# Kernel optimization log

Measured on AMD Instinct MI355X. Metric: run time of the kernel, lower is better.

Reference implementation:

```python
import jax, jax.numpy as jnp
import numpy as np

VOCAB, E, H, L, B, T, S, V = 32000, 512, 1024, 2, 64, 64, 128, 1024
LSTM_IN = 2 * E  # input_feed=True -> cat(embed, prev_output)


def setup_inputs() -> dict:
    key = jax.random.key(0)
    ks = jax.random.split(key, 12)
    s = lambda *d: 1.0 / np.sqrt(d[-1])
    return {
        "tgt_batch": jax.random.randint(ks[0], (T, B), 0, VOCAB),
        "h_encoder": jax.random.normal(ks[1], (B, S, V), jnp.float32),
        "emb": jax.random.normal(ks[2], (VOCAB, E), jnp.float32) * 0.02,
        "output_init": jnp.zeros((B, E), jnp.float32),
        "hidden_init": jnp.zeros((L, B, H), jnp.float32),
        "W_ih": jax.random.uniform(ks[3], (L, 4 * H, LSTM_IN), jnp.float32, -s(H), s(H)),
        "W_hh": jax.random.uniform(ks[4], (L, 4 * H, H), jnp.float32, -s(H), s(H)),
        "b_ih": jax.random.uniform(ks[5], (L, 4 * H), jnp.float32, -s(H), s(H)),
        "b_hh": jax.random.uniform(ks[6], (L, 4 * H), jnp.float32, -s(H), s(H)),
        "W1": jax.random.uniform(ks[7], (V, H), jnp.float32, -s(H), s(H)),   # query_size->values_size
        "b1": jnp.zeros((V,), jnp.float32),
        "W2": jax.random.uniform(ks[8], (E, H + V), jnp.float32, -s(H + V), s(H + V)),
        "b2": jnp.zeros((E,), jnp.float32),
    }


def reference(tgt_batch, h_encoder, emb, output_init, hidden_init,
              W_ih, W_hh, b_ih, b_hh, W1, b1, W2, b2):
    x_seq = emb[tgt_batch]  # [T, B, E]

    def lstm_cell(x, h, c):  # x:[B,2E], h/c:[L,B,H]
        hs, cs, inp = [], [], x
        for l in range(L):
            gates = inp @ W_ih[l].T + b_ih[l] + h[l] @ W_hh[l].T + b_hh[l]
            i, f, g, o = jnp.split(gates, 4, axis=-1)  # torch gate order i,f,g,o
            c_new = jax.nn.sigmoid(f) * c[l] + jax.nn.sigmoid(i) * jnp.tanh(g)
            h_new = jax.nn.sigmoid(o) * jnp.tanh(c_new)
            hs.append(h_new); cs.append(c_new); inp = h_new
        return jnp.stack(hs), jnp.stack(cs), inp

    def global_attn(query):  # query:[B,H]
        q = query @ W1.T + b1                              # [B,V]
        scores = jnp.einsum('bv,bsv->bs', q, h_encoder)    # [B,S]
        a = jax.nn.softmax(scores, axis=-1)
        attended = jnp.einsum('bs,bsv->bv', a, h_encoder)  # [B,V]
        return jnp.tanh(jnp.concatenate([attended, query], axis=-1) @ W2.T + b2)

    def step(carry, x):
        h, c, out = carry
        inp = jnp.concatenate([x, out], axis=-1)  # input feed
        h, c, top = lstm_cell(inp, h, c)
        o = global_attn(top)  # dropout is identity in eval mode
        return (h, c, o), o

    c0 = jnp.zeros_like(hidden_init)
    _, outs = jax.lax.scan(step, (hidden_init, c0, output_init), x_seq)
    return jnp.transpose(outs, (1, 0, 2))  # [B, T, E]
```

## Files before the change

kernel.cpp:

```cpp
#include <hip/hip_runtime.h>

typedef _Float16 f16;
typedef f16 f16x8 __attribute__((ext_vector_type(8)));
typedef f16 f16x2 __attribute__((ext_vector_type(2)));
typedef float f32x4 __attribute__((ext_vector_type(4)));
typedef unsigned long long u64;

#define MFMA16(a, b, c) __builtin_amdgcn_mfma_f32_16x16x32_f16(a, b, c, 0, 0, 0)
#define ROT 16

__device__ inline float fsig(float x) { return 1.f / (1.f + __expf(-x)); }
__device__ inline float ftanh(float x) {
    x = fminf(15.f, fmaxf(-15.f, x));
    float e = __expf(2.f * x);
    return (e - 1.f) / (e + 1.f);
}

__device__ __forceinline__ void bstore8(void* p, u64 v) {
    __hip_atomic_store((u64*)p, v, __ATOMIC_RELAXED, __HIP_MEMORY_SCOPE_AGENT);
}
__device__ __forceinline__ void bstore4(float* p, float v) {
    __hip_atomic_store(p, v, __ATOMIC_RELAXED, __HIP_MEMORY_SCOPE_AGENT);
}
__device__ __forceinline__ float bload_f32(const float* p) {
    return __hip_atomic_load((float*)p, __ATOMIC_RELAXED, __HIP_MEMORY_SCOPE_AGENT);
}

__global__ __launch_bounds__(256) void k_convert(
    const float* __restrict__ Wih, const float* __restrict__ Whh,
    const float* __restrict__ W1, const float* __restrict__ W2,
    const float* __restrict__ bih, const float* __restrict__ bhh,
    const int* __restrict__ tgt, const float* __restrict__ emb,
    const float* __restrict__ henc,
    f16* __restrict__ wcat, f16* __restrict__ w1c, f16* __restrict__ w2a,
    f16* __restrict__ w2b, float* __restrict__ bsum, f16* __restrict__ Xall,
    f16* __restrict__ h16)
{
    const long NW = 16777216, NT = 1048576, NA = 524288, NB = 524288,
               NS = 8192, NX = 2097152, NH = 8388608;
    const long TOT = NW + NT + NA + NB + NS + NX + NH;
    for (long i = (long)blockIdx.x * 256 + threadIdx.x; i < TOT;
         i += (long)gridDim.x * 256) {
        if (i < NW) {
            long l = i >> 23;
            long r = i & 8388607;
            int j = (int)(r >> 11), k = (int)(r & 2047);
            float val = (k < 1024) ? Wih[(l * 4096 + j) * 1024 + k]
                                   : Whh[(l * 4096 + j) * 1024 + (k - 1024)];
            wcat[i] = (f16)val;
        } else if (i < NW + NT) {
            long r = i - NW;
            int h = (int)(r >> 10), v = (int)(r & 1023);
            w1c[r] = (f16)W1[(long)v * 1024 + h];
        } else if (i < NW + NT + NA) {
            long r = i - NW - NT;
            int e = (int)(r >> 10), v = (int)(r & 1023);
            w2a[r] = (f16)W2[(long)e * 2048 + v];
        } else if (i < NW + NT + NA + NB) {
            long r = i - NW - NT - NA;
            int e = (int)(r >> 10), k = (int)(r & 1023);
            w2b[r] = (f16)W2[(long)e * 2048 + 1024 + k];
        } else if (i < NW + NT + NA + NB + NS) {
            long r = i - NW - NT - NA - NB;
            bsum[r] = bih[r] + bhh[r];
        } else if (i < NW + NT + NA + NB + NS + NX) {
            long r = i - NW - NT - NA - NB - NS;
            int t = (int)(r >> 15), mm = (int)((r >> 9) & 63), k = (int)(r & 511);
            Xall[r] = (f16)emb[(long)tgt[t * 64 + mm] * 512 + k];
        } else {
            long r = i - NW - NT - NA - NB - NS - NX;
            h16[r] = (f16)henc[r];
        }
    }
}

__global__ __launch_bounds__(256) void k_init(
    const float* __restrict__ oinit, const float* __restrict__ hinit,
    f16* __restrict__ O0, f16* __restrict__ H00, f16* __restrict__ H10,
    float* __restrict__ c01, unsigned* __restrict__ sync)
{
    int idx = blockIdx.x * 256 + threadIdx.x;
    if (idx < 32768) {
        O0[idx] = (f16)oinit[idx];
    } else if (idx < 98304) {
        H00[idx - 32768] = (f16)hinit[idx - 32768];
    } else if (idx < 163840) {
        H10[idx - 98304] = (f16)hinit[65536 + (idx - 98304)];
    } else if (idx < 294912) {
        c01[idx - 163840] = 0.f;
    } else if (idx < 297984) {
        sync[idx - 294912] = 0u;
    }
}

__global__ __launch_bounds__(256) void k_sb(
    const float* __restrict__ b1, const float* __restrict__ henc,
    float* __restrict__ sb)
{
    int bs = blockIdx.x * 256 + threadIdx.x;
    const float* hr = henc + (long)bs * 1024;
    float a = 0.f;
    for (int k = 0; k < 1024; k += 4) {
        float4 h4 = *(const float4*)(hr + k);
        float4 b4 = *(const float4*)(b1 + k);
        a += h4.x * b4.x + h4.y * b4.y + h4.z * b4.z + h4.w * b4.w;
    }
    sb[bs] = a;
}

__global__ __launch_bounds__(256) void k_gemm(
    const f16* __restrict__ A, const f16* __restrict__ Bm,
    f16* __restrict__ C, int N)
{
    int nb = N >> 7;
    int bm = blockIdx.x / nb, bn = blockIdx.x % nb;
    int tid = threadIdx.x, w = tid >> 6, lane = tid & 63;
    int quad = lane >> 4, nn = lane & 15;
    const f16* ap = A + (long)(bm * 64 + w * 16 + nn) * 1024 + quad * 8;
    const f16* bp = Bm + (long)(bn * 128 + nn) * 1024 + quad * 8;
    f32x4 acc[8] = {};
    for (int kk = 0; kk < 1024; kk += 32) {
        f16x8 av = *(const f16x8*)(ap + kk);
        #pragma unroll
        for (int t2 = 0; t2 < 8; ++t2) {
            f16x8 bv = *(const f16x8*)(bp + (long)t2 * 16 * 1024 + kk);
            acc[t2] = MFMA16(av, bv, acc[t2]);
        }
    }
    #pragma unroll
    for (int t2 = 0; t2 < 8; ++t2)
        #pragma unroll
        for (int r = 0; r < 4; ++r) {
            int m = bm * 64 + w * 16 + quad * 4 + r;
            int col = bn * 128 + t2 * 16 + nn;
            C[(long)m * N + col] = (f16)acc[t2][r];
        }
}

__device__ __forceinline__ void gsync(unsigned* sync, unsigned e) {
    asm volatile("s_waitcnt vmcnt(0) lgkmcnt(0)" ::: "memory");
    __syncthreads();
    if (threadIdx.x == 0) {
        int g = blockIdx.x & 7;
        unsigned* arr = sync + 32 * g;
        unsigned* rel = sync + 256 + 32 * g;
        unsigned* mst = sync + 512;
        unsigned old = __hip_atomic_fetch_add(arr, 1u, __ATOMIC_RELAXED,
                                              __HIP_MEMORY_SCOPE_AGENT);
        if (old == e * 32u - 1u) {
            unsigned old2 = __hip_atomic_fetch_add(mst, 1u, __ATOMIC_RELAXED,
                                                   __HIP_MEMORY_SCOPE_AGENT);
            if (old2 == e * 8u - 1u) {
                #pragma unroll
                for (int g2 = 0; g2 < 8; ++g2)
                    __hip_atomic_store(sync + 256 + 32 * g2, e, __ATOMIC_RELAXED,
                                       __HIP_MEMORY_SCOPE_AGENT);
            }
        }
        while (__hip_atomic_fetch_add(rel, 0u, __ATOMIC_RELAXED,
                                      __HIP_MEMORY_SCOPE_AGENT) < e)
            __builtin_amdgcn_s_sleep(2);
    }
    __syncthreads();
    asm volatile("" ::: "memory");
}

__device__ __forceinline__ void lstm_core(
    const f16* base, int rst, const f16x8* wreg,
    const float* __restrict__ bs_, float* __restrict__ c_,
    f16* __restrict__ dest, float* lds, int b, int tid)
{
    int w = tid >> 6, lane = tid & 63, quad = lane >> 4, n = lane & 15;
    const f16* ap = base + (long)n * rst + quad * 8;
    f32x4 acc0 = {}, acc1 = {}, acc2 = {}, acc3 = {};
    #pragma unroll
    for (int kk = 0; kk < 8; ++kk) {
        f16x8 bv = wreg[kk];
        f16x8 a0 = *(const f16x8*)(ap + kk * 32);
        f16x8 a1 = *(const f16x8*)(ap + (long)16 * rst + kk * 32);
        f16x8 a2 = *(const f16x8*)(ap + (long)32 * rst + kk * 32);
        f16x8 a3 = *(const f16x8*)(ap + (long)48 * rst + kk * 32);
        acc0 = MFMA16(a0, bv, acc0);
        acc1 = MFMA16(a1, bv, acc1);
        acc2 = MFMA16(a2, bv, acc2);
        acc3 = MFMA16(a3, bv, acc3);
    }
    #pragma unroll
    for (int r = 0; r < 4; ++r) {
        int mb = quad * 4 + r;
        lds[(w * 64 + mb) * 17 + n]      = acc0[r];
        lds[(w * 64 + 16 + mb) * 17 + n] = acc1[r];
        lds[(w * 64 + 32 + mb) * 17 + n] = acc2[r];
        lds[(w * 64 + 48 + mb) * 17 + n] = acc3[r];
    }
    __syncthreads();
    if (tid < 256) {
        int m = tid >> 2, uu = tid & 3;
        float s0 = 0.f, s1 = 0.f, s2 = 0.f, s3 = 0.f;
        #pragma unroll
        for (int ww = 0; ww < 8; ++ww) {
            const float* p = lds + (ww * 64 + m) * 17 + uu * 4;
            s0 += p[0]; s1 += p[1]; s2 += p[2]; s3 += p[3];
        }
        int ug = b * 4 + uu;
        float iv = fsig(s0 + bs_[ug]);
        float fv = fsig(s1 + bs_[1024 + ug]);
        float gv = ftanh(s2 + bs_[2048 + ug]);
        float ov = fsig(s3 + bs_[3072 + ug]);
        float cold = c_[m * 1024 + ug];
        float cn = fv * cold + iv * gv;
        float hn = ov * ftanh(cn);
        c_[m * 1024 + ug] = cn;
        lds[8704 + m * 4 + uu] = hn;
    }
    __syncthreads();
    if (tid < 64) {
        union { f16 h[4]; u64 u; } pk;
        #pragma unroll
        for (int uu = 0; uu < 4; ++uu) pk.h[uu] = (f16)lds[8704 + tid * 4 + uu];
        bstore8(dest + (long)tid * 1024 + b * 4, pk.u);
    }
}

__device__ __forceinline__ void z1_core(
    const f16* __restrict__ H1n, const f16x8* wz, const float* __restrict__ b2,
    float* __restrict__ Z1f, int bb, int khalf, float* lds, int tid)
{
    int w = tid >> 6, lane = tid & 63, quad = lane >> 4, n = lane & 15;
    const f16* ap = H1n + (long)n * 1024 + khalf * 512 + w * 64 + quad * 8;
    f32x4 acc0 = {}, acc1 = {}, acc2 = {}, acc3 = {};
    #pragma unroll
    for (int kk = 0; kk < 2; ++kk) {
        f16x8 bv = wz[kk];
        f16x8 a0 = *(const f16x8*)(ap + kk * 32);
        f16x8 a1 = *(const f16x8*)(ap + 16384 + kk * 32);
        f16x8 a2 = *(const f16x8*)(ap + 32768 + kk * 32);
        f16x8 a3 = *(const f16x8*)(ap + 49152 + kk * 32);
        acc0 = MFMA16(a0, bv, acc0);
        acc1 = MFMA16(a1, bv, acc1);
        acc2 = MFMA16(a2, bv, acc2);
        acc3 = MFMA16(a3, bv, acc3);
    }
    #pragma unroll
    for (int r = 0; r < 4; ++r) {
        int mb = quad * 4 + r;
        lds[(w * 64 + mb) * 17 + n]      = acc0[r];
        lds[(w * 64 + 16 + mb) * 17 + n] = acc1[r];
        lds[(w * 64 + 32 + mb) * 17 + n] = acc2[r];
        lds[(w * 64 + 48 + mb) * 17 + n] = acc3[r];
    }
    __syncthreads();
    int m = tid >> 3, n0 = (tid & 7) * 2;
    float s0 = 0.f, s1 = 0.f;
    #pragma unroll
    for (int ww = 0; ww < 8; ++ww) {
        const float* p = lds + (ww * 64 + m) * 17 + n0;
        s0 += p[0]; s1 += p[1];
    }
    int e = bb * 16 + n0;
    if (khalf == 0) { s0 += b2[e]; s1 += b2[e + 1]; }
    union { float f[2]; u64 u; } pk;
    pk.f[0] = s0; pk.f[1] = s1;
    bstore8(Z1f + khalf * 32768 + (long)m * 512 + e, pk.u);
}

__global__ __launch_bounds__(512, 2) void k_persist(
    const f16* __restrict__ wcat, const float* __restrict__ bsum,
    float* __restrict__ c01, const f16* __restrict__ Xall,
    f16* __restrict__ Orot, f16* __restrict__ H0rot, f16* __restrict__ H1rot,
    const f16* __restrict__ P16, const f16* __restrict__ Q216,
    const f16* __restrict__ w2b, const float* __restrict__ sb,
    const float* __restrict__ b2, float* __restrict__ out,
    float* __restrict__ Z1f, float* __restrict__ Z2p,
    float* __restrict__ Sc, unsigned* __restrict__ sync)
{
    extern __shared__ float smem[];
    float* scr = smem;
    f16* Pl  = (f16*)(smem + 8960);
    f16* Q2l = Pl + 32768;

    int b = blockIdx.x, tid = threadIdx.x;
    int m = b >> 2, sq = b & 3;
    int wv = tid >> 6, lane = tid & 63, quad = lane >> 4, nn = lane & 15;
    unsigned* cnt = sync + 1024;

    f16x8 w0[8], w1[8];
    {
        int j0 = (nn & 3) * 1024 + b * 4 + (nn >> 2);
        const f16* wp = wcat + (long)j0 * 2048 + wv * 256 + quad * 8;
        #pragma unroll
        for (int kk = 0; kk < 8; ++kk) {
            w0[kk] = *(const f16x8*)(wp + kk * 32);
            w1[kk] = *(const f16x8*)(wp + 8388608 + kk * 32);
        }
    }
    f16x8 wz[2];
    if (b >= 64 && b < 128) {
        int zb = b - 64, bb = zb & 31, kh = zb >> 5;
        int j = bb * 16 + nn;
        const f16* zp = w2b + (long)j * 1024 + kh * 512 + wv * 64 + quad * 8;
        #pragma unroll
        for (int kk = 0; kk < 2; ++kk) wz[kk] = *(const f16x8*)(zp + kk * 32);
    }
    {
        const uint4* gp = (const uint4*)(P16 + ((long)(m * 128 + sq * 32)) * 1024);
        #pragma unroll
        for (int i = 0; i < 8; ++i) ((uint4*)Pl)[i * 512 + tid] = gp[i * 512 + tid];
        const uint4* gq = (const uint4*)(Q216 + ((long)(m * 128 + sq * 32)) * 512);
        #pragma unroll
        for (int i = 0; i < 4; ++i) ((uint4*)Q2l)[i * 512 + tid] = gq[i * 512 + tid];
    }
    __syncthreads();

    unsigned epoch = 0;
    for (int t = 0; t < 64; ++t) {
        int rs0 = t & (ROT - 1), rs1 = (t + 1) & (ROT - 1);
        const f16* Xc = Xall + (long)t * 32768;
        const f16* Oc = Orot + (long)rs0 * 32768;
        const f16* H0c = H0rot + (long)rs0 * 65536;
        f16* H0n = H0rot + (long)rs1 * 65536;
        const f16* H1c = H1rot + (long)rs0 * 65536;
        f16* H1n = H1rot + (long)rs1 * 65536;

        {
            const f16* base; int rst;
            if (wv < 2)      { base = Xc + wv * 256;        rst = 512; }
            else if (wv < 4) { base = Oc + (wv - 2) * 256;  rst = 512; }
            else             { base = H0c + (wv - 4) * 256; rst = 1024; }
            lstm_core(base, rst, w0, bsum, c01, H0n, scr, b, tid);
        }
        gsync(sync, ++epoch);

        {
            const f16* base = (wv < 4) ? (H0n + wv * 256) : (H1c + (wv - 4) * 256);
            lstm_core(base, 1024, w1, bsum + 4096, c01 + 65536, H1n, scr, b, tid);
        }
        gsync(sync, ++epoch);

        {
            f16* h1l = (f16*)scr;
            if (tid < 128)
                ((uint4*)h1l)[tid] = *(const uint4*)(H1n + (long)m * 1024 + tid * 8);
            __syncthreads();
            int sl = tid >> 4, kc = tid & 15;
            const f16* prow = Pl + sl * 1024;
            float a0 = 0.f;
            #pragma unroll
            for (int i = 0; i < 8; ++i) {
                int ch = (i * 16 + kc) * 8;
                f16x8 pv = *(const f16x8*)(prow + ch);
                f16x8 hv = *(const f16x8*)(h1l + ch);
                #pragma unroll
                for (int p2 = 0; p2 < 4; ++p2) {
                    f16x2 pa = { pv[p2 * 2], pv[p2 * 2 + 1] };
                    f16x2 ha = { hv[p2 * 2], hv[p2 * 2 + 1] };
                    a0 = __builtin_amdgcn_fdot2(pa, ha, a0, false);
                }
            }
            #pragma unroll
            for (int off = 8; off; off >>= 1) a0 += __shfl_xor(a0, off, 16);
            if (kc == 0)
                bstore4(Sc + m * 128 + sq * 32 + sl, a0 + sb[m * 128 + sq * 32 + sl]);
            __syncthreads();
            if (b >= 64 && b < 128)
                z1_core(H1n, wz, b2, Z1f, (b - 64) & 31, (b - 64) >> 5, scr, tid);
        }
        gsync(sync, ++epoch);

        {
            if (tid < 128) scr[tid] = bload_f32(Sc + m * 128 + tid);
            __syncthreads();
            if (tid < 64) {
                float v = fmaxf(scr[tid], scr[64 + tid]);
                #pragma unroll
                for (int off = 32; off; off >>= 1) v = fmaxf(v, __shfl_down(v, off));
                if (tid == 0) scr[128] = v;
            }
            __syncthreads();
            if (tid < 128) scr[tid] = __expf(scr[tid] - scr[128]);
            __syncthreads();
            if (tid < 64) {
                float v = scr[tid] + scr[64 + tid];
                #pragma unroll
                for (int off = 32; off; off >>= 1) v += __shfl_down(v, off);
                if (tid == 0) scr[129] = 1.f / v;
            }
            __syncthreads();
            float inv = scr[129];
            float zp = 0.f;
            #pragma unroll 8
            for (int jy = 0; jy < 32; ++jy)
                zp += scr[sq * 32 + jy] * (float)Q2l[jy * 512 + tid];
            bstore4(Z2p + ((m * 4 + sq) << 9) + tid, zp * inv);
            asm volatile("s_waitcnt vmcnt(0)" ::: "memory");
            __syncthreads();
            if (tid == 0) {
                unsigned old = __hip_atomic_fetch_add(cnt + m * 32, 1u,
                        __ATOMIC_RELAXED, __HIP_MEMORY_SCOPE_AGENT);
                scr[130] = (old == (unsigned)(4 * t + 3)) ? 1.f : 0.f;
            }
            __syncthreads();
            if (scr[130] != 0.f) {
                float z = bload_f32(Z1f + (m << 9) + tid)
                        + bload_f32(Z1f + 32768 + (m << 9) + tid);
                #pragma unroll
                for (int q = 0; q < 4; ++q)
                    z += bload_f32(Z2p + ((m * 4 + q) << 9) + tid);
                float o = ftanh(z);
                out[((long)m * 64 + t) * 512 + tid] = o;
                f16* ob = (f16*)(scr + 192);
                ob[tid] = (f16)o;
                __syncthreads();
                if (tid < 128) {
                    union { f16 h[4]; u64 u; } pk;
                    #pragma unroll
                    for (int i = 0; i < 4; ++i) pk.h[i] = ob[tid * 4 + i];
                    bstore8(Orot + (long)rs1 * 32768 + m * 512 + tid * 4, pk.u);
                }
            }
        }
        gsync(sync, ++epoch);
    }
}

extern "C" void kernel_launch(void* const* d_in, const int* in_sizes, int n_in,
                              void* d_out, int out_size, void* d_ws, size_t ws_size,
                              hipStream_t stream)
{
    const int*   tgt   = (const int*)d_in[0];
    const float* henc  = (const float*)d_in[1];
    const float* emb   = (const float*)d_in[2];
    const float* oinit = (const float*)d_in[3];
    const float* hinit = (const float*)d_in[4];
    const float* Wih   = (const float*)d_in[5];
    const float* Whh   = (const float*)d_in[6];
    const float* bih   = (const float*)d_in[7];
    const float* bhh   = (const float*)d_in[8];
    const float* W1    = (const float*)d_in[9];
    const float* b1    = (const float*)d_in[10];
    const float* W2    = (const float*)d_in[11];
    const float* b2    = (const float*)d_in[12];
    float* out = (float*)d_out;

    char* ws = (char*)d_ws;
    f16*      wcat  = (f16*)(ws + 0);
    f16*      P16   = (f16*)(ws + 33554432);
    f16*      Q216  = (f16*)(ws + 50331648);
    f16*      h16   = (f16*)(ws + 58720256);
    f16*      w2b   = (f16*)(ws + 75497472);
    f16*      w1c   = (f16*)(ws + 76546048);
    f16*      w2a   = (f16*)(ws + 78643200);
    f16*      Xall  = (f16*)(ws + 79691776);
    f16*      H0rot = (f16*)(ws + 83886080);
    f16*      H1rot = (f16*)(ws + 85983232);
    f16*      Orot  = (f16*)(ws + 88080384);
    float*    c01   = (float*)(ws + 89128960);
    float*    Z1f   = (float*)(ws + 89653248);
    float*    Z2p   = (float*)(ws + 89915392);
    float*    Sc    = (float*)(ws + 90439680);
    float*    bsum  = (float*)(ws + 90472448);
    float*    sb    = (float*)(ws + 90505216);
    unsigned* sync  = (unsigned*)(ws + 90537984);

    hipLaunchKernelGGL(k_convert, dim3(4096), dim3(256), 0, stream,
                       Wih, Whh, W1, W2, bih, bhh, tgt, emb, henc,
                       wcat, w1c, w2a, w2b, bsum, Xall, h16);
    hipLaunchKernelGGL(k_init, dim3(1164), dim3(256), 0, stream,
                       oinit, hinit, Orot, H0rot, H1rot, c01, sync);
    hipLaunchKernelGGL(k_sb, dim3(32), dim3(256), 0, stream, b1, henc, sb);
    hipLaunchKernelGGL(k_gemm, dim3(128 * 8), dim3(256), 0, stream,
                       h16, w1c, P16, 1024);
    hipLaunchKernelGGL(k_gemm, dim3(128 * 4), dim3(256), 0, stream,
                       h16, w2a, Q216, 512);

    static const unsigned LDS_BYTES = 8960 * 4 + 32768 * 2 + 16384 * 2;
    hipFuncSetAttribute((const void*)k_persist,
                        hipFuncAttributeMaxDynamicSharedMemorySize, LDS_BYTES);
    void* args[] = { &wcat, &bsum, &c01, &Xall, &Orot, &H0rot, &H1rot, &P16,
                     &Q216, &w2b, &sb, &b2, &out, &Z1f, &Z2p, &Sc, &sync };
    hipLaunchCooperativeKernel((const void*)k_persist, dim3(256), dim3(512),
                               args, LDS_BYTES, stream);
}
```

Measured before the change: 2.449 ms.

## Replace grid-wide barriers with fine-grained per-block dataflow flags

Removes the hierarchical global barrier (gsync) used four times per timestep. Each block now publishes an epoch flag after finishing a stage, and only the waves that consume that data poll the producers they depend on. The layer-0 input-feed waves wait on per-row output flags, the layer-1 waves on all layer-0 flags, the attention and z1 stages on layer-1 flags, and the softmax stage on only its four score blocks. This cuts barrier latency and lets independent work overlap across stages. In exchange it relies on relaxed atomics plus vmcnt waits for ordering and on the ring-buffer depth to avoid write-after-read hazards, which raises the risk of subtle races.

After: 3.257 ms. +33.0%, slower.

```diff
diff --git a/kernel.cpp b/kernel.cpp
--- a/kernel.cpp
+++ b/kernel.cpp
@@ -24,6 +24,40 @@
 }
 __device__ __forceinline__ float bload_f32(const float* p) {
     return __hip_atomic_load((float*)p, __ATOMIC_RELAXED, __HIP_MEMORY_SCOPE_AGENT);
+}
+__device__ __forceinline__ void fstore_u32(unsigned* p, unsigned v) {
+    __hip_atomic_store(p, v, __ATOMIC_RELAXED, __HIP_MEMORY_SCOPE_AGENT);
+}
+__device__ __forceinline__ unsigned fload_u32(unsigned* p) {
+    return __hip_atomic_load(p, __ATOMIC_RELAXED, __HIP_MEMORY_SCOPE_AGENT);
+}
+
+__device__ __forceinline__ void poll256(unsigned* f, unsigned e, int lane) {
+    for (;;) {
+        unsigned v0 = fload_u32(f + lane);
+        unsigned v1 = fload_u32(f + 64 + lane);
+        unsigned v2 = fload_u32(f + 128 + lane);
+        unsigned v3 = fload_u32(f + 192 + lane);
+        if (__all((int)(v0 >= e && v1 >= e && v2 >= e && v3 >= e))) break;
+        __builtin_amdgcn_s_sleep(2);
+    }
+    asm volatile("" ::: "memory");
+}
+__device__ __forceinline__ void poll64x(unsigned* f, unsigned e, int lane) {
+    for (;;) {
+        unsigned v = fload_u32(f + lane);
+        if (__all((int)(v >= e))) break;
+        __builtin_amdgcn_s_sleep(2);
+    }
+    asm volatile("" ::: "memory");
+}
+__device__ __forceinline__ void poll4(unsigned* f, unsigned e, int lane) {
+    for (;;) {
+        unsigned v = fload_u32(f + (lane & 3));
+        if (__all((int)(v >= e))) break;
+        __builtin_amdgcn_s_sleep(1);
+    }
+    asm volatile("" ::: "memory");
 }
 
 __global__ __launch_bounds__(256) void k_convert(
@@ -137,34 +171,6 @@
         }
 }
 
-__device__ __forceinline__ void gsync(unsigned* sync, unsigned e) {
-    asm volatile("s_waitcnt vmcnt(0) lgkmcnt(0)" ::: "memory");
-    __syncthreads();
-    if (threadIdx.x == 0) {
-        int g = blockIdx.x & 7;
-        unsigned* arr = sync + 32 * g;
-        unsigned* rel = sync + 256 + 32 * g;
-        unsigned* mst = sync + 512;
-        unsigned old = __hip_atomic_fetch_add(arr, 1u, __ATOMIC_RELAXED,
-                                              __HIP_MEMORY_SCOPE_AGENT);
-        if (old == e * 32u - 1u) {
-            unsigned old2 = __hip_atomic_fetch_add(mst, 1u, __ATOMIC_RELAXED,
-                                                   __HIP_MEMORY_SCOPE_AGENT);
-            if (old2 == e * 8u - 1u) {
-                #pragma unroll
-                for (int g2 = 0; g2 < 8; ++g2)
-                    __hip_atomic_store(sync + 256 + 32 * g2, e, __ATOMIC_RELAXED,
-                                       __HIP_MEMORY_SCOPE_AGENT);
-            }
-        }
-        while (__hip_atomic_fetch_add(rel, 0u, __ATOMIC_RELAXED,
-                                      __HIP_MEMORY_SCOPE_AGENT) < e)
-            __builtin_amdgcn_s_sleep(2);
-    }
-    __syncthreads();
-    asm volatile("" ::: "memory");
-}
-
 __device__ __forceinline__ void lstm_core(
     const f16* base, int rst, const f16x8* wreg,
     const float* __restrict__ bs_, float* __restrict__ c_,
@@ -282,7 +288,15 @@
     int b = blockIdx.x, tid = threadIdx.x;
     int m = b >> 2, sq = b & 3;
     int wv = tid >> 6, lane = tid & 63, quad = lane >> 4, nn = lane & 15;
-    unsigned* cnt = sync + 1024;
+
+    unsigned* bflagA = sync;
+    unsigned* bflagB = sync + 256;
+    unsigned* sflag  = sync + 512;
+    unsigned* zflag  = sync + 768;
+    unsigned* oflag  = sync + 832;
+    unsigned* cnt    = sync + 1024;
+
+    const bool zb = (b >= 64 && b < 128);
 
     f16x8 w0[8], w1[8];
     {
@@ -295,8 +309,8 @@
         }
     }
     f16x8 wz[2];
-    if (b >= 64 && b < 128) {
-        int zb = b - 64, bb = zb & 31, kh = zb >> 5;
+    if (zb) {
+        int zz = b - 64, bb = zz & 31, kh = zz >> 5;
         int j = bb * 16 + nn;
         const f16* zp = w2b + (long)j * 1024 + kh * 512 + wv * 64 + quad * 8;
         #pragma unroll
@@ -312,7 +326,6 @@
     }
     __syncthreads();
 
-    unsigned epoch = 0;
     for (int t = 0; t < 64; ++t) {
         int rs0 = t & (ROT - 1), rs1 = (t + 1) & (ROT - 1);
         const f16* Xc = Xall + (long)t * 32768;
@@ -325,19 +338,35 @@
         {
             const f16* base; int rst;
             if (wv < 2)      { base = Xc + wv * 256;        rst = 512; }
-            else if (wv < 4) { base = Oc + (wv - 2) * 256;  rst = 512; }
+            else if (wv < 4) {
+                poll64x(oflag, (unsigned)t, lane);
+                base = Oc + (wv - 2) * 256;  rst = 512;
+            }
             else             { base = H0c + (wv - 4) * 256; rst = 1024; }
             lstm_core(base, rst, w0, bsum, c01, H0n, scr, b, tid);
         }
-        gsync(sync, ++epoch);
+        if (wv == 0) {
+            asm volatile("s_waitcnt vmcnt(0)" ::: "memory");
+            if (tid == 0) fstore_u32(bflagA + b, (unsigned)(t + 1));
+        }
 
         {
-            const f16* base = (wv < 4) ? (H0n + wv * 256) : (H1c + (wv - 4) * 256);
+            const f16* base;
+            if (wv < 4) {
+                poll256(bflagA, (unsigned)(t + 1), lane);
+                base = H0n + wv * 256;
+            } else {
+                base = H1c + (wv - 4) * 256;
+            }
             lstm_core(base, 1024, w1, bsum + 4096, c01 + 65536, H1n, scr, b, tid);
         }
-        gsync(sync, ++epoch);
+        if (wv == 0) {
+            asm volatile("s_waitcnt vmcnt(0)" ::: "memory");
+            if (tid == 0) fstore_u32(bflagB + b, (unsigned)(t + 1));
+        }
 
         {
+            if (wv < 2 || zb) poll256(bflagB, (unsigned)(t + 1), lane);
             f16* h1l = (f16*)scr;
             if (tid < 128)
                 ((uint4*)h1l)[tid] = *(const uint4*)(H1n + (long)m * 1024 + tid * 8);
@@ -361,13 +390,19 @@
             for (int off = 8; off; off >>= 1) a0 += __shfl_xor(a0, off, 16);
             if (kc == 0)
                 bstore4(Sc + m * 128 + sq * 32 + sl, a0 + sb[m * 128 + sq * 32 + sl]);
-            __syncthreads();
-            if (b >= 64 && b < 128)
+            asm volatile("s_waitcnt vmcnt(0)" ::: "memory");
+            __syncthreads();
+            if (tid == 0) fstore_u32(sflag + b, (unsigned)(t + 1));
+            if (zb) {
                 z1_core(H1n, wz, b2, Z1f, (b - 64) & 31, (b - 64) >> 5, scr, tid);
-        }
-        gsync(sync, ++epoch);
+                asm volatile("s_waitcnt vmcnt(0)" ::: "memory");
+                __syncthreads();
+                if (tid == 0) fstore_u32(zflag + (b - 64), (unsigned)(t + 1));
+            }
+        }
 
         {
+            if (wv < 2) poll4(sflag + m * 4, (unsigned)(t + 1), lane);
             if (tid < 128) scr[tid] = bload_f32(Sc + m * 128 + tid);
             __syncthreads();
             if (tid < 64) {
@@ -400,7 +435,11 @@
                 scr[130] = (old == (unsigned)(4 * t + 3)) ? 1.f : 0.f;
             }
             __syncthreads();
-            if (scr[130] != 0.f) {
+            float win = scr[130];
+            __syncthreads();
+            if (win != 0.f) {
+                if (wv == 0) poll64x(zflag, (unsigned)(t + 1), lane);
+                __syncthreads();
                 float z = bload_f32(Z1f + (m << 9) + tid)
                         + bload_f32(Z1f + 32768 + (m << 9) + tid);
                 #pragma unroll
@@ -417,9 +456,11 @@
                     for (int i = 0; i < 4; ++i) pk.h[i] = ob[tid * 4 + i];
                     bstore8(Orot + (long)rs1 * 32768 + m * 512 + tid * 4, pk.u);
                 }
-            }
-        }
-        gsync(sync, ++epoch);
+                if (wv < 2) asm volatile("s_waitcnt vmcnt(0)" ::: "memory");
+                __syncthreads();
+                if (tid == 0) fstore_u32(oflag + m, (unsigned)(t + 1));
+            }
+        }
     }
 }
 
```
